# Kernel tuning notes

Hardware: AMD Instinct MI355X
Metric: run time of the kernel (lower is better)

Reference implementation:

```python
import jax, jax.numpy as jnp
import numpy as np

H = 256          # hidden_dim
T = 3            # number of agent types (hard-coded in module)
N = 24576        # total agents, contiguous by type
N3 = N // T      # agents per type


def _ln(x, s, b):
    mu = jnp.mean(x, -1, keepdims=True)
    v = jnp.var(x, -1, keepdims=True)
    return (x - mu) * jax.lax.rsqrt(v + 1e-5) * s + b


def setup_inputs() -> dict:
    key = jax.random.key(0)
    ks = jax.random.split(key, 20)
    def p(i, shape, scale=0.02):
        return jax.random.normal(ks[i], shape, jnp.float32) * scale
    inp = {}
    inp['agent_x'] = p(0, (N, H), 1.0)
    inp['lane_x'] = p(1, (N, H), 1.0)
    inp['poly_x'] = p(2, (N, H), 1.0)
    inp['l2a_src'] = jax.random.randint(ks[3], (N,), 0, N)
    inp['g2a_src'] = jax.random.randint(ks[4], (N,), 0, N)
    # other_src[s, d] = src agent of type s for dst agent d (types contiguous)
    inp['other_src'] = jax.random.randint(ks[5], (T, N), 0, N3) + (jnp.arange(T) * N3)[:, None]
    # per-agent-type params
    inp['self_W'] = p(6, (T, H, H)); inp['self_b'] = jnp.zeros((T, H))
    inp['out_W'] = p(7, (T, 4 * H, H)); inp['out_b'] = jnp.zeros((T, H))
    inp['ffn_ln_s'] = jnp.ones((T, H)); inp['ffn_ln_b'] = jnp.zeros((T, H))
    inp['ffn_w1'] = p(8, (T, H, 4 * H)); inp['ffn_b1'] = jnp.zeros((T, 4 * H))
    inp['ffn_w2'] = p(9, (T, 4 * H, H)); inp['ffn_b2'] = jnp.zeros((T, H))
    inp['ffn_w3'] = p(10, (T, H, 4 * H)); inp['ffn_b3'] = jnp.zeros((T, 4 * H))
    # shared edge MLPs (prenorm: LN -> w1 -> relu -> w2)
    inp['l2a_ln_s'] = jnp.ones((3 * H,)); inp['l2a_ln_b'] = jnp.zeros((3 * H,))
    inp['l2a_w1'] = p(11, (3 * H, 4 * H)); inp['l2a_b1'] = jnp.zeros((4 * H,))
    inp['l2a_w2'] = p(12, (4 * H, H)); inp['l2a_b2'] = jnp.zeros((H,))
    inp['g2a_ln_s'] = jnp.ones((2 * H,)); inp['g2a_ln_b'] = jnp.zeros((2 * H,))
    inp['g2a_w1'] = p(13, (2 * H, 4 * H)); inp['g2a_b1'] = jnp.zeros((4 * H,))
    inp['g2a_w2'] = p(14, (4 * H, H)); inp['g2a_b2'] = jnp.zeros((H,))
    # per-src-agent-type 'other' MLPs
    inp['oth_ln_s'] = jnp.ones((T, 3 * H)); inp['oth_ln_b'] = jnp.zeros((T, 3 * H))
    inp['oth_w1'] = p(15, (T, 3 * H, 4 * H)); inp['oth_b1'] = jnp.zeros((T, 4 * H))
    inp['oth_w2'] = p(16, (T, 4 * H, H)); inp['oth_b2'] = jnp.zeros((T, H))
    return inp


def reference(agent_x, lane_x, poly_x, self_W, self_b, out_W, out_b,
              ffn_ln_s, ffn_ln_b, ffn_w1, ffn_b1, ffn_w2, ffn_b2, ffn_w3, ffn_b3,
              l2a_ln_s, l2a_ln_b, l2a_w1, l2a_b1, l2a_w2, l2a_b2,
              g2a_ln_s, g2a_ln_b, g2a_w1, g2a_b1, g2a_w2, g2a_b2,
              oth_ln_s, oth_ln_b, oth_w1, oth_b1, oth_w2, oth_b2,
              l2a_src, g2a_src, other_src):
    x = agent_x.reshape(T, N3, H)                      # agents grouped by type
    # self branch: Linear + ReLU per type
    self_out = jax.nn.relu(jnp.einsum('tnh,thk->tnk', x, self_W) + self_b[:, None, :])
    # l2a edge MLP: cat([lane, agent, lane]) -> prenorm MLP (shared weights)
    lane_feat = lane_x[l2a_src].reshape(T, N3, H)
    l2a_in = jnp.concatenate([lane_feat, x, lane_feat], -1)      # [T,N3,3H]
    l2a_out = jax.nn.relu(_ln(l2a_in, l2a_ln_s, l2a_ln_b) @ l2a_w1 + l2a_b1) @ l2a_w2 + l2a_b2
    # g2a edge MLP: cat([polygon, agent])
    poly_feat = poly_x[g2a_src].reshape(T, N3, H)
    g2a_in = jnp.concatenate([poly_feat, x], -1)                 # [T,N3,2H]
    g2a_out = jax.nn.relu(_ln(g2a_in, g2a_ln_s, g2a_ln_b) @ g2a_w1 + g2a_b1) @ g2a_w2 + g2a_b2
    # agent-other-agent: per source-agent-type MLP, then aggregate over src types
    src_feat = agent_x[other_src].reshape(T, T, N3, H)           # [src_t, dst_t, N3, H]
    xb = jnp.broadcast_to(x[None], (T, T, N3, H))
    oth_in = jnp.concatenate([src_feat, xb, src_feat], -1)       # [s,t,n,3H]
    oth_n = _ln(oth_in, oth_ln_s[:, None, None, :], oth_ln_b[:, None, None, :])
    oth_h = jax.nn.relu(jnp.einsum('stnd,sdm->stnm', oth_n, oth_w1) + oth_b1[:, None, None, :])
    oth_out = jnp.einsum('stnm,smh->stnh', oth_h, oth_w2) + oth_b2[:, None, None, :]
    other_agg = oth_out.sum(0)                                   # [T,N3,H]
    # fuse 4 branches -> out_fc -> PositionwiseFeedForward -> residual
    fused = jnp.concatenate([self_out, l2a_out, g2a_out, other_agg], -1)  # [T,N3,4H]
    out = jnp.einsum('tnd,tdh->tnh', fused, out_W) + out_b[:, None, :]
    y = _ln(out, ffn_ln_s[:, None, :], ffn_ln_b[:, None, :])
    g = jax.nn.silu(jnp.einsum('tnh,thm->tnm', y, ffn_w1) + ffn_b1[:, None, :])
    u = jnp.einsum('tnh,thm->tnm', y, ffn_w3) + ffn_b3[:, None, :]
    out = out + jnp.einsum('tnm,tmh->tnh', g * u, ffn_w2) + ffn_b2[:, None, :]
    return (out + x).reshape(N, H)
```

## Files before the change

kernel.cpp:

```cpp
#include <hip/hip_runtime.h>
#include <hip/hip_bf16.h>

typedef __hip_bfloat16 bf16;
typedef __bf16 v8bf __attribute__((ext_vector_type(8)));
typedef float f32x4 __attribute__((ext_vector_type(4)));

#define N_AG 24576
#define N3 8192

struct __align__(8) bf4 { bf16 x, y, z, w; };
__device__ __forceinline__ bf4 mk4(float a, float b, float c, float d) {
  bf4 r{__float2bfloat16(a), __float2bfloat16(b), __float2bfloat16(c), __float2bfloat16(d)};
  return r;
}

enum {
  EPI_RELU_BIAS = 0,
  EPI_BIAS      = 1,
  EPI_ACC_INIT  = 2,
  EPI_ACC_ADD   = 3,
  EPI_FINAL     = 4,
  EPI_SILU      = 5,
  EPI_MUL       = 6,
  EPI_GLU       = 7
};

__device__ __forceinline__ void gl_lds16(const bf16* g, short* l) {
  __builtin_amdgcn_global_load_lds(
      (const __attribute__((address_space(1))) unsigned int*)g,
      (__attribute__((address_space(3))) unsigned int*)l, 16, 0, 0);
}

template<int EPI>
__device__ __forceinline__
void gemm_body(const bf16* __restrict__ A, int lda,
               const bf16* __restrict__ Bt, int ldb,
               const float* __restrict__ bias,
               float* __restrict__ accbuf,
               bf16* __restrict__ Cout, int ldc,
               const float* __restrict__ resid,
               float* __restrict__ CoutF,
               const bf16* __restrict__ gin,
               int K, int Nc, int row0, int col0)
{
  __shared__ __align__(16) short As[2][128 * 32];
  __shared__ __align__(16) short Bs[2][128 * 32];

  const int tid  = threadIdx.x;
  const int lane = tid & 63;
  const int w    = tid >> 6;
  const int quad = lane >> 4;
  const int l15  = lane & 15;

  f32x4 acc[4][4];
  const f32x4 zero = {0.f, 0.f, 0.f, 0.f};
#pragma unroll
  for (int i = 0; i < 4; ++i)
#pragma unroll
    for (int j = 0; j < 4; ++j) acc[i][j] = zero;

  const int srow = (w << 5) + (lane >> 2);
  const int ss   = ((lane >> 2) & 3) ^ ((lane >> 4) & 1);
  const int sc   = ((lane & 3) ^ ss) << 3;
  const bf16* aG = A  + (long)(row0 + srow) * lda + sc;
  const bf16* bG = Bt + (long)(col0 + srow) * ldb + sc;
  const int ldsOff = w * 1024;

  const int wr = (w >> 1) * 64;
  const int wc = (w & 1) * 64;
  const int fs = (l15 & 3) ^ ((l15 >> 2) & 1);

  gl_lds16(aG,                  As[0] + ldsOff);
  gl_lds16(aG + (long)16 * lda, As[0] + ldsOff + 512);
  gl_lds16(bG,                  Bs[0] + ldsOff);
  gl_lds16(bG + (long)16 * ldb, Bs[0] + ldsOff + 512);
  __syncthreads();

  int cur = 0;
  for (int k0 = 0; k0 < K; k0 += 32) {
    const int nk = k0 + 32;
    if (nk < K) {
      short* An = As[cur ^ 1] + ldsOff;
      short* Bn = Bs[cur ^ 1] + ldsOff;
      gl_lds16(aG + nk,                  An);
      gl_lds16(aG + nk + (long)16 * lda, An + 512);
      gl_lds16(bG + nk,                  Bn);
      gl_lds16(bG + nk + (long)16 * ldb, Bn + 512);
    }
    const short* Ac = As[cur];
    const short* Bc = Bs[cur];
    const int pc = (quad ^ fs) * 8;
    v8bf af[4], bfm[4];
#pragma unroll
    for (int i = 0; i < 4; ++i) {
      af[i]  = *(const v8bf*)&Ac[(wr + i * 16 + l15) * 32 + pc];
      bfm[i] = *(const v8bf*)&Bc[(wc + i * 16 + l15) * 32 + pc];
    }
#pragma unroll
    for (int i = 0; i < 4; ++i)
#pragma unroll
      for (int j = 0; j < 4; ++j)
        acc[i][j] = __builtin_amdgcn_mfma_f32_16x16x32_bf16(af[i], bfm[j], acc[i][j], 0, 0, 0);
    __syncthreads();
    cur ^= 1;
  }

  if constexpr (EPI == EPI_GLU) {
#pragma unroll
    for (int ct = 0; ct < 4; ct += 2) {
      const int colg = col0 + wc + ct * 16 + l15;
      const int hcol = ((colg >> 5) << 4) + (colg & 15);
      const float bg = bias[colg];
      const float bu = bias[colg + 16];
#pragma unroll
      for (int rt = 0; rt < 4; ++rt) {
#pragma unroll
        for (int i = 0; i < 4; ++i) {
          const int row = row0 + wr + rt * 16 + quad * 4 + i;
          const float vg = acc[rt][ct][i] + bg;
          const float vu = acc[rt][ct + 1][i] + bu;
          Cout[(long)row * ldc + hcol] =
              __float2bfloat16(vg / (1.f + expf(-vg)) * vu);
        }
      }
    }
  } else {
#pragma unroll
    for (int ct = 0; ct < 4; ++ct) {
      const int col = col0 + wc + ct * 16 + l15;
      const float bv = bias ? bias[col] : 0.f;
#pragma unroll
      for (int rt = 0; rt < 4; ++rt) {
#pragma unroll
        for (int i = 0; i < 4; ++i) {
          const int row = row0 + wr + rt * 16 + quad * 4 + i;
          float v = acc[rt][ct][i] + bv;
          if constexpr (EPI == EPI_RELU_BIAS) {
            Cout[(long)row * ldc + col] = __float2bfloat16(v > 0.f ? v : 0.f);
          } else if constexpr (EPI == EPI_BIAS) {
            Cout[(long)row * ldc + col] = __float2bfloat16(v);
          } else if constexpr (EPI == EPI_ACC_INIT) {
            accbuf[(long)row * Nc + col] = v;
          } else if constexpr (EPI == EPI_ACC_ADD) {
            accbuf[(long)row * Nc + col] += v;
          } else if constexpr (EPI == EPI_FINAL) {
            CoutF[(long)row * ldc + col] =
                accbuf[(long)row * Nc + col] + v + resid[(long)row * ldc + col];
          } else if constexpr (EPI == EPI_SILU) {
            Cout[(long)row * ldc + col] = __float2bfloat16(v / (1.f + expf(-v)));
          } else {
            const float g = __bfloat162float(gin[(long)row * ldc + col]);
            Cout[(long)row * ldc + col] = __float2bfloat16(v * g);
          }
        }
      }
    }
  }
}

template<int EPI>
__global__ __launch_bounds__(256)
void gemm_k(const bf16* __restrict__ A, int lda,
            const bf16* __restrict__ Bt, int ldb, long bTs,
            const float* __restrict__ bias, long biasTs,
            float* __restrict__ accbuf,
            bf16* __restrict__ Cout, int ldc,
            const float* __restrict__ resid,
            float* __restrict__ CoutF,
            const bf16* __restrict__ gin,
            int K, int Nc)
{
  const int row0 = blockIdx.x * 128;
  const int col0 = blockIdx.y * 128;
  const int t    = row0 >> 13;
  gemm_body<EPI>(A, lda, Bt + (long)t * bTs, ldb,
                 bias ? bias + (long)t * biasTs : nullptr,
                 accbuf, Cout, ldc, resid, CoutF, gin, K, Nc, row0, col0);
}

__global__ __launch_bounds__(256)
void w2m_k(const bf16* __restrict__ outwT, const bf16* __restrict__ w2c,
           bf16* __restrict__ w2m)
{
  const int z = blockIdx.z, b = z / 3, t = z % 3;
  const int j = (b == 0) ? 1 : (b == 1) ? 2 : 3;
  gemm_body<EPI_BIAS>(outwT + (long)t * 262144 + j * 256, 1024,
                      w2c + (long)b * 262144, 256,
                      nullptr, nullptr, w2m + (long)z * 262144, 1024,
                      nullptr, nullptr, nullptr, 256, 1024,
                      blockIdx.x * 128, blockIdx.y * 128);
}

__global__ __launch_bounds__(256)
void transpose_k(const float* __restrict__ src, bf16* __restrict__ dst,
                 int K, int Nc, long sB, long dB)
{
  __shared__ bf16 tile[32][33];
  const int b = blockIdx.z;
  const float* s = src + (long)b * sB;
  bf16* d = dst + (long)b * dB;
  const int kb = blockIdx.y * 32, nb = blockIdx.x * 32;
  const int tx = threadIdx.x & 31, ty = threadIdx.x >> 5;
#pragma unroll
  for (int i = 0; i < 32; i += 8)
    tile[ty + i][tx] = __float2bfloat16(s[(long)(kb + ty + i) * Nc + nb + tx]);
  __syncthreads();
#pragma unroll
  for (int i = 0; i < 32; i += 8)
    d[(long)(nb + ty + i) * K + kb + tx] = tile[tx][ty + i];
}

__global__ __launch_bounds__(256)
void transpose13_k(const float* __restrict__ w1, const float* __restrict__ w3,
                   bf16* __restrict__ dst)
{
  __shared__ bf16 tile[32][33];
  const int t  = blockIdx.z;
  const int n0 = blockIdx.x * 32;
  const int k0 = blockIdx.y * 32;
  const int gi = n0 >> 5;
  const int tx = threadIdx.x & 31, ty = threadIdx.x >> 5;
  const float* src = ((tx & 16) ? w3 : w1) + (long)t * 262144;
  const int c = 16 * gi + (tx & 15);
#pragma unroll
  for (int i = 0; i < 32; i += 8)
    tile[ty + i][tx] = __float2bfloat16(src[(long)(k0 + ty + i) * 1024 + c]);
  __syncthreads();
#pragma unroll
  for (int i = 0; i < 32; i += 8)
    dst[((long)t * 2048 + n0 + ty + i) * 256 + k0 + tx] = tile[tx][ty + i];
}

struct FoldP { const float* w1[5]; const float* ls[5]; };
__global__ __launch_bounds__(256)
void fold_w1_k(FoldP p, bf16* __restrict__ dst)
{
  __shared__ float tile[32][33];
  const int z = blockIdx.z;
  const float* w1 = p.w1[z];
  const float* ls = p.ls[z];
  bf16* d = dst + (long)z * 524288;
  const int n0 = blockIdx.x * 32, i0 = blockIdx.y * 32;
  const int tx = threadIdx.x & 31, ty = threadIdx.x >> 5;
  const bool three = (z != 1) && (i0 < 256);
#pragma unroll
  for (int ii = 0; ii < 32; ii += 8) {
    const int row = i0 + ty + ii;
    float v = ls[row] * w1[(long)row * 1024 + n0 + tx];
    if (three) v += ls[row + 512] * w1[(long)(row + 512) * 1024 + n0 + tx];
    tile[ty + ii][tx] = v;
  }
  __syncthreads();
#pragma unroll
  for (int ii = 0; ii < 32; ii += 8)
    d[(long)(n0 + ty + ii) * 512 + i0 + tx] = __float2bfloat16(tile[tx][ty + ii]);
}

struct BInitP { const float* b1[5]; const float* fb1; const float* fb3; };
__global__ __launch_bounds__(256)
void binit_k(BInitP p, float* __restrict__ B1F,
             const float* __restrict__ out_b, float* __restrict__ TB,
             float* __restrict__ B13)
{
  const int i = blockIdx.x * 256 + threadIdx.x;
  if (i < 5120) {
    B1F[i] = p.b1[i >> 10][i & 1023];
  } else if (i < 5888) {
    TB[i - 5120] = out_b[i - 5120];
  } else if (i < 12032) {
    const int idx = i - 5888;
    const int t = idx >> 11, n = idx & 2047;
    const int c = ((n >> 5) << 4) | (n & 15);
    B13[idx] = (n & 16) ? p.fb3[t * 1024 + c] : p.fb1[t * 1024 + c];
  }
}

struct B1P { const float* w1[5]; const float* lb[5]; int kin[5]; };
__global__ __launch_bounds__(256)
void b1f_add_k(B1P p, float* __restrict__ dst)
{
  const int z   = blockIdx.x;
  const int kin = p.kin[z];
  const int kpb = (kin + 31) >> 5;
  const int k0  = blockIdx.y * kpb;
  const int k1  = min(k0 + kpb, kin);
  const float* w1 = p.w1[z];
  const float* lb = p.lb[z];
  const int n = threadIdx.x;
  float a0 = 0.f, a1 = 0.f, a2 = 0.f, a3 = 0.f;
  for (int k = k0; k < k1; ++k) {
    const float l = lb[k];
    const float* row = w1 + (long)k * 1024;
    a0 += l * row[n];       a1 += l * row[n + 256];
    a2 += l * row[n + 512]; a3 += l * row[n + 768];
  }
  float* d = dst + z * 1024 + n;
  atomicAdd(d, a0);       atomicAdd(d + 256, a1);
  atomicAdd(d + 512, a2); atomicAdd(d + 768, a3);
}

__global__ __launch_bounds__(256)
void tbias_add_k(const float* __restrict__ outW,
                 const float* __restrict__ l2a_b2, const float* __restrict__ g2a_b2,
                 const float* __restrict__ oth_b2, float* __restrict__ dst)
{
  const int t = blockIdx.x, h = threadIdx.x;
  const float* W = outW + (long)t * 262144;
  const int c0 = blockIdx.y * 32;
  float acc = 0.f;
  for (int c = c0; c < c0 + 32; ++c) {
    acc += l2a_b2[c] * W[(256 + c) * 256 + h];
    acc += g2a_b2[c] * W[(512 + c) * 256 + h];
    acc += (oth_b2[c] + oth_b2[256 + c] + oth_b2[512 + c]) * W[(768 + c) * 256 + h];
  }
  atomicAdd(&dst[t * 256 + h], acc);
}

__global__ __launch_bounds__(256)
void cast_k(const float* __restrict__ src, bf16* __restrict__ dst)
{
  const long i = (long)blockIdx.x * 256 + threadIdx.x;
  const float4 v = ((const float4*)src)[i];
  ((bf4*)dst)[i] = mk4(v.x, v.y, v.z, v.w);
}

__device__ __forceinline__ void wave_reduce2(float& s, float& q) {
#pragma unroll
  for (int off = 32; off > 0; off >>= 1) {
    s += __shfl_xor(s, off, 64);
    q += __shfl_xor(q, off, 64);
  }
}

template<int THREE>
__global__ __launch_bounds__(256)
void ln_norm_k(const float* __restrict__ feat, const float* __restrict__ x,
               const int* __restrict__ srcIdx, bf16* __restrict__ out)
{
  const int w = threadIdx.x >> 6, lane = threadIdx.x & 63;
  const int r = blockIdx.x * 4 + w;
  const int src = srcIdx[r];
  const float4 f4 = ((const float4*)(feat + (long)src * 256))[lane];
  const float4 x4 = ((const float4*)(x + (long)r * 256))[lane];
  const float fw = THREE ? 2.f : 1.f;
  float s = fw * (f4.x + f4.y + f4.z + f4.w) + (x4.x + x4.y + x4.z + x4.w);
  float q = fw * (f4.x * f4.x + f4.y * f4.y + f4.z * f4.z + f4.w * f4.w) +
            (x4.x * x4.x + x4.y * x4.y + x4.z * x4.z + x4.w * x4.w);
  wave_reduce2(s, q);
  const float rD  = THREE ? (1.f / 768.f) : (1.f / 512.f);
  const float mu  = s * rD;
  const float var = q * rD - mu * mu;
  const float inv = rsqrtf(var + 1e-5f);
  bf4* o = (bf4*)(out + (long)r * 512);
  o[lane]      = mk4((f4.x - mu) * inv, (f4.y - mu) * inv,
                     (f4.z - mu) * inv, (f4.w - mu) * inv);
  o[64 + lane] = mk4((x4.x - mu) * inv, (x4.y - mu) * inv,
                     (x4.z - mu) * inv, (x4.w - mu) * inv);
}

__global__ __launch_bounds__(256)
void ln_cat3_k(const float* __restrict__ feat, const float* __restrict__ x,
               const int* __restrict__ srcIdx,
               const float* __restrict__ ls, const float* __restrict__ lb,
               bf16* __restrict__ out)
{
  const int w = threadIdx.x >> 6, lane = threadIdx.x & 63;
  const int r = blockIdx.x * 4 + w;
  const int src = srcIdx[r];
  const float4 f4 = ((const float4*)(feat + (long)src * 256))[lane];
  const float4 x4 = ((const float4*)(x + (long)r * 256))[lane];
  float s = 2.f * (f4.x + f4.y + f4.z + f4.w) + (x4.x + x4.y + x4.z + x4.w);
  float q = 2.f * (f4.x * f4.x + f4.y * f4.y + f4.z * f4.z + f4.w * f4.w) +
            (x4.x * x4.x + x4.y * x4.y + x4.z * x4.z + x4.w * x4.w);
  wave_reduce2(s, q);
  const float mu  = s * (1.f / 768.f);
  const float var = q * (1.f / 768.f) - mu * mu;
  const float inv = rsqrtf(var + 1e-5f);
  const float4 s0 = ((const float4*)ls)[lane],         b0 = ((const float4*)lb)[lane];
  const float4 s1 = ((const float4*)(ls + 256))[lane], b1 = ((const float4*)(lb + 256))[lane];
  const float4 s2 = ((const float4*)(ls + 512))[lane], b2 = ((const float4*)(lb + 512))[lane];
  bf4* o = (bf4*)(out + (long)r * 768);
  o[lane] = mk4((f4.x - mu) * inv * s0.x + b0.x, (f4.y - mu) * inv * s0.y + b0.y,
                (f4.z - mu) * inv * s0.z + b0.z, (f4.w - mu) * inv * s0.w + b0.w);
  o[64 + lane] = mk4((x4.x - mu) * inv * s1.x + b1.x, (x4.y - mu) * inv * s1.y + b1.y,
                     (x4.z - mu) * inv * s1.z + b1.z, (x4.w - mu) * inv * s1.w + b1.w);
  o[128 + lane] = mk4((f4.x - mu) * inv * s2.x + b2.x, (f4.y - mu) * inv * s2.y + b2.y,
                      (f4.z - mu) * inv * s2.z + b2.z, (f4.w - mu) * inv * s2.w + b2.w);
}

__global__ __launch_bounds__(256)
void ln_cat2_k(const float* __restrict__ feat, const float* __restrict__ x,
               const int* __restrict__ srcIdx,
               const float* __restrict__ ls, const float* __restrict__ lb,
               bf16* __restrict__ out)
{
  const int w = threadIdx.x >> 6, lane = threadIdx.x & 63;
  const int r = blockIdx.x * 4 + w;
  const int src = srcIdx[r];
  const float4 f4 = ((const float4*)(feat + (long)src * 256))[lane];
  const float4 x4 = ((const float4*)(x + (long)r * 256))[lane];
  float s = (f4.x + f4.y + f4.z + f4.w) + (x4.x + x4.y + x4.z + x4.w);
  float q = (f4.x * f4.x + f4.y * f4.y + f4.z * f4.z + f4.w * f4.w) +
            (x4.x * x4.x + x4.y * x4.y + x4.z * x4.z + x4.w * x4.w);
  wave_reduce2(s, q);
  const float mu  = s * (1.f / 512.f);
  const float var = q * (1.f / 512.f) - mu * mu;
  const float inv = rsqrtf(var + 1e-5f);
  const float4 s0 = ((const float4*)ls)[lane],         b0 = ((const float4*)lb)[lane];
  const float4 s1 = ((const float4*)(ls + 256))[lane], b1 = ((const float4*)(lb + 256))[lane];
  bf4* o = (bf4*)(out + (long)r * 512);
  o[lane] = mk4((f4.x - mu) * inv * s0.x + b0.x, (f4.y - mu) * inv * s0.y + b0.y,
                (f4.z - mu) * inv * s0.z + b0.z, (f4.w - mu) * inv * s0.w + b0.w);
  o[64 + lane] = mk4((x4.x - mu) * inv * s1.x + b1.x, (x4.y - mu) * inv * s1.y + b1.y,
                     (x4.z - mu) * inv * s1.z + b1.z, (x4.w - mu) * inv * s1.w + b1.w);
}

__global__ __launch_bounds__(256)
void ln_ffn_k(const float* __restrict__ ob, const float* __restrict__ ls,
              const float* __restrict__ lb, bf16* __restrict__ y, long lsStride)
{
  const int w = threadIdx.x >> 6, lane = threadIdx.x & 63;
  const int r = blockIdx.x * 4 + w;
  const long po = (long)(r >> 13) * lsStride;
  const float4 v4 = ((const float4*)(ob + (long)r * 256))[lane];
  float s = v4.x + v4.y + v4.z + v4.w;
  float q = v4.x * v4.x + v4.y * v4.y + v4.z * v4.z + v4.w * v4.w;
  wave_reduce2(s, q);
  const float mu  = s * (1.f / 256.f);
  const float var = q * (1.f / 256.f) - mu * mu;
  const float inv = rsqrtf(var + 1e-5f);
  const float4 s0 = ((const float4*)(ls + po))[lane];
  const float4 b0 = ((const float4*)(lb + po))[lane];
  ((bf4*)(y + (long)r * 256))[lane] =
      mk4((v4.x - mu) * inv * s0.x + b0.x, (v4.y - mu) * inv * s0.y + b0.y,
          (v4.z - mu) * inv * s0.z + b0.z, (v4.w - mu) * inv * s0.w + b0.w);
}

__global__ __launch_bounds__(256)
void silu_mul_k(bf16* __restrict__ g, const bf16* __restrict__ u)
{
  const long i = (long)blockIdx.x * 256 + threadIdx.x;
  const bf4 g4 = ((const bf4*)g)[i];
  const bf4 u4 = ((const bf4*)u)[i];
  float a = __bfloat162float(g4.x), b = __bfloat162float(g4.y);
  float c = __bfloat162float(g4.z), d = __bfloat162float(g4.w);
  a = a / (1.f + expf(-a)) * __bfloat162float(u4.x);
  b = b / (1.f + expf(-b)) * __bfloat162float(u4.y);
  c = c / (1.f + expf(-c)) * __bfloat162float(u4.z);
  d = d / (1.f + expf(-d)) * __bfloat162float(u4.w);
  ((bf4*)g)[i] = mk4(a, b, c, d);
}

__global__ __launch_bounds__(256)
void fill_k(float* __restrict__ p, int n)
{
  const int i = blockIdx.x * 256 + threadIdx.x;
  if (i < n) p[i] = 2.0f;
}

extern "C" void kernel_launch(void* const* d_in, const int* in_sizes, int n_in,
                              void* d_out, int out_size, void* d_ws, size_t ws_size,
                              hipStream_t stream)
{
  const float* agent_x  = (const float*)d_in[0];
  const float* lane_x   = (const float*)d_in[1];
  const float* poly_x   = (const float*)d_in[2];
  const int*   l2a_src  = (const int*)d_in[3];
  const int*   g2a_src  = (const int*)d_in[4];
  const int*   other_src= (const int*)d_in[5];
  const float* self_W   = (const float*)d_in[6];
  const float* self_b   = (const float*)d_in[7];
  const float* out_W    = (const float*)d_in[8];
  const float* out_b    = (const float*)d_in[9];
  const float* ffn_ln_s = (const float*)d_in[10];
  const float* ffn_ln_b = (const float*)d_in[11];
  const float* ffn_w1   = (const float*)d_in[12];
  const float* ffn_b1   = (const float*)d_in[13];
  const float* ffn_w2   = (const float*)d_in[14];
  const float* ffn_b2   = (const float*)d_in[15];
  const float* ffn_w3   = (const float*)d_in[16];
  const float* ffn_b3   = (const float*)d_in[17];
  const float* l2a_ln_s = (const float*)d_in[18];
  const float* l2a_ln_b = (const float*)d_in[19];
  const float* l2a_w1   = (const float*)d_in[20];
  const float* l2a_b1   = (const float*)d_in[21];
  const float* l2a_w2   = (const float*)d_in[22];
  const float* l2a_b2   = (const float*)d_in[23];
  const float* g2a_ln_s = (const float*)d_in[24];
  const float* g2a_ln_b = (const float*)d_in[25];
  const float* g2a_w1   = (const float*)d_in[26];
  const float* g2a_b1   = (const float*)d_in[27];
  const float* g2a_w2   = (const float*)d_in[28];
  const float* g2a_b2   = (const float*)d_in[29];
  const float* oth_ln_s = (const float*)d_in[30];
  const float* oth_ln_b = (const float*)d_in[31];
  const float* oth_w1   = (const float*)d_in[32];
  const float* oth_b1   = (const float*)d_in[33];
  const float* oth_w2   = (const float*)d_in[34];
  const float* oth_b2   = (const float*)d_in[35];

  float* outp = (float*)d_out;
  const dim3 B256(256);

  const size_t TIER_A = 135707648;
  const size_t TIER_C = 12058624;

  if (ws_size >= TIER_A) {
    char* base = (char*)d_ws;
    bf16* wT = (bf16*)base;
    const long SELF_WT = 0,       OUT_WT  = 196608,  FFN_W13T = 983040;
    const long FFN_W2T = 2555904;
    const long W2C = 3342336,     W1F     = 4653056, W2M      = 7274496;
    float* B1F  = (float*)(base + 22413312L);
    float* TB   = (float*)(base + 22433792L);
    float* B13  = (float*)(base + 22436864L);
    bf16*  nbuf = (bf16*)(base + 22461440L);
    bf16*  h1   = (bf16*)(base + 47627264L);
    float* oF   = (float*)(base + 97958912L);
    bf16*  ybuf = (bf16*)(base + 123124736L);
    bf16*  xbf  = h1;

    auto TRB = [&](const float* s, long dOff, int K, int Nc, long sB, long dB, int b) {
      transpose_k<<<dim3(Nc / 32, K / 32, b), B256, 0, stream>>>(s, wT + dOff, K, Nc, sB, dB);
    };
    TRB(self_W, SELF_WT, 256, 256,  65536, 65536, 3);
    TRB(out_W,  OUT_WT,  1024, 256, 262144, 262144, 3);
    TRB(ffn_w2, FFN_W2T, 1024, 256, 262144, 262144, 3);
    transpose13_k<<<dim3(64, 8, 3), B256, 0, stream>>>(ffn_w1, ffn_w3, wT + FFN_W13T);
    cast_k<<<256, B256, 0, stream>>>(l2a_w2, wT + W2C);
    cast_k<<<256, B256, 0, stream>>>(g2a_w2, wT + W2C + 262144);
    cast_k<<<768, B256, 0, stream>>>(oth_w2, wT + W2C + 524288);

    FoldP fp = {{l2a_w1, g2a_w1, oth_w1, oth_w1 + 786432, oth_w1 + 1572864},
                {l2a_ln_s, g2a_ln_s, oth_ln_s, oth_ln_s + 768, oth_ln_s + 1536}};
    fold_w1_k<<<dim3(32, 16, 5), B256, 0, stream>>>(fp, wT + W1F);

    BInitP ip = {{l2a_b1, g2a_b1, oth_b1, oth_b1 + 1024, oth_b1 + 2048}, ffn_b1, ffn_b3};
    binit_k<<<47, B256, 0, stream>>>(ip, B1F, out_b, TB, B13);
    B1P bp = {{l2a_w1, g2a_w1, oth_w1, oth_w1 + 786432, oth_w1 + 1572864},
              {l2a_ln_b, g2a_ln_b, oth_ln_b, oth_ln_b + 768, oth_ln_b + 1536},
              {768, 512, 768, 768, 768}};
    b1f_add_k<<<dim3(5, 32), B256, 0, stream>>>(bp, B1F);
    tbias_add_k<<<dim3(3, 8), B256, 0, stream>>>(out_W, l2a_b2, g2a_b2, oth_b2, TB);
    w2m_k<<<dim3(2, 8, 15), B256, 0, stream>>>(wT + OUT_WT, wT + W2C, wT + W2M);

    const dim3 Gw1(N_AG / 128, 8), Gw2(N_AG / 128, 2), Gglu(N_AG / 128, 16);

    cast_k<<<N_AG / 4, B256, 0, stream>>>(agent_x, xbf);
    gemm_k<EPI_RELU_BIAS><<<Gw2, B256, 0, stream>>>(
        xbf, 256, wT + SELF_WT, 256, 65536, self_b, 256,
        nullptr, ybuf, 256, nullptr, nullptr, nullptr, 256, 256);
    gemm_k<EPI_ACC_INIT><<<Gw2, B256, 0, stream>>>(
        ybuf, 256, wT + OUT_WT, 1024, 262144, TB, 256,
        oF, nullptr, 0, nullptr, nullptr, nullptr, 256, 256);

    for (int b = 0; b < 5; ++b) {
      const int* src = (b == 0) ? l2a_src : (b == 1) ? g2a_src
                                          : other_src + (long)(b - 2) * N_AG;
      const float* feat = (b == 0) ? lane_x : (b == 1) ? poly_x : agent_x;
      if (b == 1) ln_norm_k<0><<<N_AG / 4, B256, 0, stream>>>(feat, agent_x, src, nbuf);
      else        ln_norm_k<1><<<N_AG / 4, B256, 0, stream>>>(feat, agent_x, src, nbuf);
      gemm_k<EPI_RELU_BIAS><<<Gw1, B256, 0, stream>>>(
          nbuf, 512, wT + W1F + (long)b * 524288, 512, 0, B1F + b * 1024, 0,
          nullptr, h1, 1024, nullptr, nullptr, nullptr, 512, 1024);
      gemm_k<EPI_ACC_ADD><<<Gw2, B256, 0, stream>>>(
          h1, 1024, wT + W2M + (long)b * 786432, 1024, 262144, nullptr, 0,
          oF, nullptr, 0, nullptr, nullptr, nullptr, 1024, 256);
    }

    ln_ffn_k<<<N_AG / 4, B256, 0, stream>>>(oF, ffn_ln_s, ffn_ln_b, ybuf, 256);
    gemm_k<EPI_GLU><<<Gglu, B256, 0, stream>>>(
        ybuf, 256, wT + FFN_W13T, 256, 524288, B13, 2048,
        nullptr, h1, 1024, nullptr, nullptr, nullptr, 256, 2048);
    gemm_k<EPI_FINAL><<<Gw2, B256, 0, stream>>>(
        h1, 1024, wT + FFN_W2T, 1024, 262144, ffn_b2, 256,
        oF, nullptr, 256, agent_x, outp, nullptr, 1024, 256);
    return;
  }

  if (ws_size < TIER_C) {
    fill_k<<<(out_size + 255) / 256, B256, 0, stream>>>(outp, out_size);
    return;
  }

  const int CH = 2048;
  char* base = (char*)d_ws;
  bf16*  wt     = (bf16*)base;
  bf16*  nbuf   = (bf16*)(base + 1572864L);
  bf16*  bbuf   = (bf16*)(base + 4718592L);
  bf16*  h1     = (bf16*)(base + 5767168L);
  float* outF32 = (float*)(base + 9961472L);
  bf16*  ybuf   = (bf16*)(base + 524288L);
  bf16*  xbf    = h1;
  bf16*  g_pre  = h1;
  bf16*  u_pre  = nbuf;

  const dim3 Gw1(CH / 128, 8), Gw2(CH / 128, 2);
  auto TR = [&](const float* s, int K, int Nc) {
    transpose_k<<<dim3(Nc / 32, K / 32), B256, 0, stream>>>(s, wt, K, Nc, 0, 0);
  };

  for (int t = 0; t < 3; ++t) {
    for (int c = 0; c < N3 / CH; ++c) {
      const long r0 = (long)t * N3 + (long)c * CH;
      const float* xC   = agent_x + r0 * 256;
      float*       outC = outp + r0 * 256;

      cast_k<<<CH / 4, B256, 0, stream>>>(xC, xbf);
      TR(self_W + (long)t * 65536, 256, 256);
      gemm_k<EPI_RELU_BIAS><<<Gw2, B256, 0, stream>>>(
          xbf, 256, wt, 256, 0, self_b + t * 256, 0, nullptr, bbuf, 256,
          nullptr, nullptr, nullptr, 256, 256);
      TR(out_W + (long)t * 262144 + 0 * 65536, 256, 256);
      gemm_k<EPI_ACC_INIT><<<Gw2, B256, 0, stream>>>(
          bbuf, 256, wt, 256, 0, out_b + t * 256, 0, outF32, nullptr, 0,
          nullptr, nullptr, nullptr, 256, 256);

      ln_cat3_k<<<CH / 4, B256, 0, stream>>>(lane_x, xC, l2a_src + r0,
                                             l2a_ln_s, l2a_ln_b, nbuf);
      TR(l2a_w1, 768, 1024);
      gemm_k<EPI_RELU_BIAS><<<Gw1, B256, 0, stream>>>(
          nbuf, 768, wt, 768, 0, l2a_b1, 0, nullptr, h1, 1024,
          nullptr, nullptr, nullptr, 768, 1024);
      TR(l2a_w2, 1024, 256);
      gemm_k<EPI_BIAS><<<Gw2, B256, 0, stream>>>(
          h1, 1024, wt, 1024, 0, l2a_b2, 0, nullptr, bbuf, 256,
          nullptr, nullptr, nullptr, 1024, 256);
      TR(out_W + (long)t * 262144 + 1 * 65536, 256, 256);
      gemm_k<EPI_ACC_ADD><<<Gw2, B256, 0, stream>>>(
          bbuf, 256, wt, 256, 0, nullptr, 0, outF32, nullptr, 0,
          nullptr, nullptr, nullptr, 256, 256);

      ln_cat2_k<<<CH / 4, B256, 0, stream>>>(poly_x, xC, g2a_src + r0,
                                             g2a_ln_s, g2a_ln_b, nbuf);
      TR(g2a_w1, 512, 1024);
      gemm_k<EPI_RELU_BIAS><<<Gw1, B256, 0, stream>>>(
          nbuf, 512, wt, 512, 0, g2a_b1, 0, nullptr, h1, 1024,
          nullptr, nullptr, nullptr, 512, 1024);
      TR(g2a_w2, 1024, 256);
      gemm_k<EPI_BIAS><<<Gw2, B256, 0, stream>>>(
          h1, 1024, wt, 1024, 0, g2a_b2, 0, nullptr, bbuf, 256,
          nullptr, nullptr, nullptr, 1024, 256);
      TR(out_W + (long)t * 262144 + 2 * 65536, 256, 256);
      gemm_k<EPI_ACC_ADD><<<Gw2, B256, 0, stream>>>(
          bbuf, 256, wt, 256, 0, nullptr, 0, outF32, nullptr, 0,
          nullptr, nullptr, nullptr, 256, 256);

      for (int s = 0; s < 3; ++s) {
        ln_cat3_k<<<CH / 4, B256, 0, stream>>>(
            agent_x, xC, other_src + (long)s * N_AG + r0,
            oth_ln_s + s * 768, oth_ln_b + s * 768, nbuf);
        TR(oth_w1 + (long)s * 786432, 768, 1024);
        gemm_k<EPI_RELU_BIAS><<<Gw1, B256, 0, stream>>>(
            nbuf, 768, wt, 768, 0, oth_b1 + s * 1024, 0, nullptr, h1, 1024,
            nullptr, nullptr, nullptr, 768, 1024);
        TR(oth_w2 + (long)s * 262144, 1024, 256);
        gemm_k<EPI_BIAS><<<Gw2, B256, 0, stream>>>(
            h1, 1024, wt, 1024, 0, oth_b2 + s * 256, 0, nullptr, bbuf, 256,
            nullptr, nullptr, nullptr, 1024, 256);
        TR(out_W + (long)t * 262144 + 3 * 65536, 256, 256);
        gemm_k<EPI_ACC_ADD><<<Gw2, B256, 0, stream>>>(
            bbuf, 256, wt, 256, 0, nullptr, 0, outF32, nullptr, 0,
            nullptr, nullptr, nullptr, 256, 256);
      }

      ln_ffn_k<<<CH / 4, B256, 0, stream>>>(outF32, ffn_ln_s + t * 256,
                                            ffn_ln_b + t * 256, ybuf, 0);
      TR(ffn_w1 + (long)t * 262144, 256, 1024);
      gemm_k<EPI_BIAS><<<Gw1, B256, 0, stream>>>(
          ybuf, 256, wt, 256, 0, ffn_b1 + t * 1024, 0, nullptr, g_pre, 1024,
          nullptr, nullptr, nullptr, 256, 1024);
      TR(ffn_w3 + (long)t * 262144, 256, 1024);
      gemm_k<EPI_BIAS><<<Gw1, B256, 0, stream>>>(
          ybuf, 256, wt, 256, 0, ffn_b3 + t * 1024, 0, nullptr, u_pre, 1024,
          nullptr, nullptr, nullptr, 256, 1024);
      silu_mul_k<<<CH, B256, 0, stream>>>(g_pre, u_pre);
      TR(ffn_w2 + (long)t * 262144, 1024, 256);
      gemm_k<EPI_FINAL><<<Gw2, B256, 0, stream>>>(
          g_pre, 1024, wt, 1024, 0, ffn_b2 + t * 256, 0, outF32, nullptr, 256,
          xC, outC, nullptr, 1024, 256);
    }
  }
}
```

Before: 844.1 us.

## Split-K with atomic accumulation for narrow N=256 GEMMs

After: 1.131 ms. +34.0%, slower.

```diff
diff --git a/kernel.cpp b/kernel.cpp
--- a/kernel.cpp
+++ b/kernel.cpp
@@ -22,7 +22,8 @@
   EPI_FINAL     = 4,
   EPI_SILU      = 5,
   EPI_MUL       = 6,
-  EPI_GLU       = 7
+  EPI_GLU       = 7,
+  EPI_ACC_ATOMIC= 8
 };
 
 __device__ __forceinline__ void gl_lds16(const bf16* g, short* l) {
@@ -143,6 +144,8 @@
             accbuf[(long)row * Nc + col] = v;
           } else if constexpr (EPI == EPI_ACC_ADD) {
             accbuf[(long)row * Nc + col] += v;
+          } else if constexpr (EPI == EPI_ACC_ATOMIC) {
+            atomicAdd(&accbuf[(long)row * Nc + col], v);
           } else if constexpr (EPI == EPI_FINAL) {
             CoutF[(long)row * ldc + col] =
                 accbuf[(long)row * Nc + col] + v + resid[(long)row * ldc + col];
@@ -178,6 +181,24 @@
                  accbuf, Cout, ldc, resid, CoutF, gin, K, Nc, row0, col0);
 }
 
+template<int EPI>
+__global__ __launch_bounds__(256)
+void gemm_splitk_k(const bf16* __restrict__ A, int lda,
+                   const bf16* __restrict__ Bt, int ldb, long bTs,
+                   const float* __restrict__ bias,
+                   float* __restrict__ accbuf, int Kper, int Nc)
+{
+  const int row0 = blockIdx.x * 128;
+  const int col0 = blockIdx.y * 128;
+  const int t    = row0 >> 13;
+  const int z    = blockIdx.z;
+  gemm_body<EPI>(A + (long)z * Kper, lda,
+                 Bt + (long)t * bTs + (long)z * Kper, ldb,
+                 (z == 0) ? bias : nullptr,
+                 accbuf, nullptr, 0, nullptr, nullptr, nullptr,
+                 Kper, Nc, row0, col0);
+}
+
 __global__ __launch_bounds__(256)
 void w2m_k(const bf16* __restrict__ outwT, const bf16* __restrict__ w2c,
            bf16* __restrict__ w2m)
@@ -189,6 +210,23 @@
                       nullptr, nullptr, w2m + (long)z * 262144, 1024,
                       nullptr, nullptr, nullptr, 256, 1024,
                       blockIdx.x * 128, blockIdx.y * 128);
+}
+
+__global__ __launch_bounds__(256)
+void final_add_k(const float* __restrict__ oF, const float* __restrict__ x,
+                 const float* __restrict__ b2, float* __restrict__ out)
+{
+  const long idx = (long)blockIdx.x * 256 + threadIdx.x;
+  const long i4  = idx * 4;
+  const int  t   = (int)(i4 >> 21);
+  const int  c4  = (int)(i4 & 255) >> 2;
+  const float4 a = ((const float4*)oF)[idx];
+  const float4 r = ((const float4*)x)[idx];
+  const float4 b = ((const float4*)(b2 + t * 256))[c4];
+  float4 o;
+  o.x = a.x + b.x + r.x; o.y = a.y + b.y + r.y;
+  o.z = a.z + b.z + r.z; o.w = a.w + b.w + r.w;
+  ((float4*)out)[idx] = o;
 }
 
 __global__ __launch_bounds__(256)
@@ -545,6 +583,7 @@
     w2m_k<<<dim3(2, 8, 15), B256, 0, stream>>>(wT + OUT_WT, wT + W2C, wT + W2M);
 
     const dim3 Gw1(N_AG / 128, 8), Gw2(N_AG / 128, 2), Gglu(N_AG / 128, 16);
+    const dim3 Gks(N_AG / 128, 2, 4);
 
     cast_k<<<N_AG / 4, B256, 0, stream>>>(agent_x, xbf);
     gemm_k<EPI_RELU_BIAS><<<Gw2, B256, 0, stream>>>(
@@ -563,18 +602,18 @@
       gemm_k<EPI_RELU_BIAS><<<Gw1, B256, 0, stream>>>(
           nbuf, 512, wT + W1F + (long)b * 524288, 512, 0, B1F + b * 1024, 0,
           nullptr, h1, 1024, nullptr, nullptr, nullptr, 512, 1024);
-      gemm_k<EPI_ACC_ADD><<<Gw2, B256, 0, stream>>>(
-          h1, 1024, wT + W2M + (long)b * 786432, 1024, 262144, nullptr, 0,
-          oF, nullptr, 0, nullptr, nullptr, nullptr, 1024, 256);
+      gemm_splitk_k<EPI_ACC_ATOMIC><<<Gks, B256, 0, stream>>>(
+          h1, 1024, wT + W2M + (long)b * 786432, 1024, 262144,
+          nullptr, oF, 256, 256);
     }
 
     ln_ffn_k<<<N_AG / 4, B256, 0, stream>>>(oF, ffn_ln_s, ffn_ln_b, ybuf, 256);
     gemm_k<EPI_GLU><<<Gglu, B256, 0, stream>>>(
         ybuf, 256, wT + FFN_W13T, 256, 524288, B13, 2048,
         nullptr, h1, 1024, nullptr, nullptr, nullptr, 256, 2048);
-    gemm_k<EPI_FINAL><<<Gw2, B256, 0, stream>>>(
-        h1, 1024, wT + FFN_W2T, 1024, 262144, ffn_b2, 256,
-        oF, nullptr, 256, agent_x, outp, nullptr, 1024, 256);
+    gemm_splitk_k<EPI_ACC_ATOMIC><<<Gks, B256, 0, stream>>>(
+        h1, 1024, wT + FFN_W2T, 1024, 262144, nullptr, oF, 256, 256);
+    final_add_k<<<N_AG / 4, B256, 0, stream>>>(oF, agent_x, ffn_b2, outp);
     return;
   }
 
```

## Add 64x64-tile GEMM kernel for narrow-output GEMMs to raise block count

Applied to the files above, without the earlier changes.

After: 805.7 us. -4.5%, faster.

```diff
diff --git a/kernel.cpp b/kernel.cpp
--- a/kernel.cpp
+++ b/kernel.cpp
@@ -159,6 +159,100 @@
 }
 
 template<int EPI>
+__device__ __forceinline__
+void gemm64_body(const bf16* __restrict__ A, int lda,
+                 const bf16* __restrict__ Bt, int ldb,
+                 const float* __restrict__ bias,
+                 float* __restrict__ accbuf,
+                 bf16* __restrict__ Cout, int ldc,
+                 const float* __restrict__ resid,
+                 float* __restrict__ CoutF,
+                 int K, int Nc, int row0, int col0)
+{
+  __shared__ __align__(16) short As[2][64 * 32];
+  __shared__ __align__(16) short Bs[2][64 * 32];
+
+  const int tid  = threadIdx.x;
+  const int lane = tid & 63;
+  const int w    = tid >> 6;
+  const int quad = lane >> 4;
+  const int l15  = lane & 15;
+
+  f32x4 acc[2][2];
+  const f32x4 zero = {0.f, 0.f, 0.f, 0.f};
+#pragma unroll
+  for (int i = 0; i < 2; ++i)
+#pragma unroll
+    for (int j = 0; j < 2; ++j) acc[i][j] = zero;
+
+  const int srow = (w << 4) + (lane >> 2);
+  const int ss   = ((lane >> 2) & 3) ^ ((lane >> 4) & 1);
+  const int sc   = ((lane & 3) ^ ss) << 3;
+  const bf16* aG = A  + (long)(row0 + srow) * lda + sc;
+  const bf16* bG = Bt + (long)(col0 + srow) * ldb + sc;
+  const int ldsOff = w * 512;
+
+  const int wr = (w >> 1) * 32;
+  const int wc = (w & 1) * 32;
+  const int fs = (l15 & 3) ^ ((l15 >> 2) & 1);
+
+  gl_lds16(aG, As[0] + ldsOff);
+  gl_lds16(bG, Bs[0] + ldsOff);
+  __syncthreads();
+
+  int cur = 0;
+  for (int k0 = 0; k0 < K; k0 += 32) {
+    const int nk = k0 + 32;
+    if (nk < K) {
+      gl_lds16(aG + nk, As[cur ^ 1] + ldsOff);
+      gl_lds16(bG + nk, Bs[cur ^ 1] + ldsOff);
+    }
+    const short* Ac = As[cur];
+    const short* Bc = Bs[cur];
+    const int pc = (quad ^ fs) * 8;
+    v8bf af[2], bfm[2];
+#pragma unroll
+    for (int i = 0; i < 2; ++i) {
+      af[i]  = *(const v8bf*)&Ac[(wr + i * 16 + l15) * 32 + pc];
+      bfm[i] = *(const v8bf*)&Bc[(wc + i * 16 + l15) * 32 + pc];
+    }
+#pragma unroll
+    for (int i = 0; i < 2; ++i)
+#pragma unroll
+      for (int j = 0; j < 2; ++j)
+        acc[i][j] = __builtin_amdgcn_mfma_f32_16x16x32_bf16(af[i], bfm[j], acc[i][j], 0, 0, 0);
+    __syncthreads();
+    cur ^= 1;
+  }
+
+#pragma unroll
+  for (int ct = 0; ct < 2; ++ct) {
+    const int col = col0 + wc + ct * 16 + l15;
+    const float bv = bias ? bias[col] : 0.f;
+#pragma unroll
+    for (int rt = 0; rt < 2; ++rt) {
+#pragma unroll
+      for (int i = 0; i < 4; ++i) {
+        const int row = row0 + wr + rt * 16 + quad * 4 + i;
+        float v = acc[rt][ct][i] + bv;
+        if constexpr (EPI == EPI_RELU_BIAS) {
+          Cout[(long)row * ldc + col] = __float2bfloat16(v > 0.f ? v : 0.f);
+        } else if constexpr (EPI == EPI_BIAS) {
+          Cout[(long)row * ldc + col] = __float2bfloat16(v);
+        } else if constexpr (EPI == EPI_ACC_INIT) {
+          accbuf[(long)row * Nc + col] = v;
+        } else if constexpr (EPI == EPI_ACC_ADD) {
+          accbuf[(long)row * Nc + col] += v;
+        } else if constexpr (EPI == EPI_FINAL) {
+          CoutF[(long)row * ldc + col] =
+              accbuf[(long)row * Nc + col] + v + resid[(long)row * ldc + col];
+        }
+      }
+    }
+  }
+}
+
+template<int EPI>
 __global__ __launch_bounds__(256)
 void gemm_k(const bf16* __restrict__ A, int lda,
             const bf16* __restrict__ Bt, int ldb, long bTs,
@@ -178,17 +272,36 @@
                  accbuf, Cout, ldc, resid, CoutF, gin, K, Nc, row0, col0);
 }
 
+template<int EPI>
+__global__ __launch_bounds__(256)
+void gemm64_k(const bf16* __restrict__ A, int lda,
+              const bf16* __restrict__ Bt, int ldb, long bTs,
+              const float* __restrict__ bias, long biasTs,
+              float* __restrict__ accbuf,
+              bf16* __restrict__ Cout, int ldc,
+              const float* __restrict__ resid,
+              float* __restrict__ CoutF,
+              int K, int Nc)
+{
+  const int row0 = blockIdx.x * 64;
+  const int col0 = blockIdx.y * 64;
+  const int t    = row0 >> 13;
+  gemm64_body<EPI>(A, lda, Bt + (long)t * bTs, ldb,
+                   bias ? bias + (long)t * biasTs : nullptr,
+                   accbuf, Cout, ldc, resid, CoutF, K, Nc, row0, col0);
+}
+
 __global__ __launch_bounds__(256)
 void w2m_k(const bf16* __restrict__ outwT, const bf16* __restrict__ w2c,
            bf16* __restrict__ w2m)
 {
   const int z = blockIdx.z, b = z / 3, t = z % 3;
   const int j = (b == 0) ? 1 : (b == 1) ? 2 : 3;
-  gemm_body<EPI_BIAS>(outwT + (long)t * 262144 + j * 256, 1024,
-                      w2c + (long)b * 262144, 256,
-                      nullptr, nullptr, w2m + (long)z * 262144, 1024,
-                      nullptr, nullptr, nullptr, 256, 1024,
-                      blockIdx.x * 128, blockIdx.y * 128);
+  gemm64_body<EPI_BIAS>(outwT + (long)t * 262144 + j * 256, 1024,
+                        w2c + (long)b * 262144, 256,
+                        nullptr, nullptr, w2m + (long)z * 262144, 1024,
+                        nullptr, nullptr, 256, 1024,
+                        blockIdx.x * 64, blockIdx.y * 64);
 }
 
 __global__ __launch_bounds__(256)
@@ -542,17 +655,18 @@
               {768, 512, 768, 768, 768}};
     b1f_add_k<<<dim3(5, 32), B256, 0, stream>>>(bp, B1F);
     tbias_add_k<<<dim3(3, 8), B256, 0, stream>>>(out_W, l2a_b2, g2a_b2, oth_b2, TB);
-    w2m_k<<<dim3(2, 8, 15), B256, 0, stream>>>(wT + OUT_WT, wT + W2C, wT + W2M);
-
-    const dim3 Gw1(N_AG / 128, 8), Gw2(N_AG / 128, 2), Gglu(N_AG / 128, 16);
+    w2m_k<<<dim3(4, 16, 15), B256, 0, stream>>>(wT + OUT_WT, wT + W2C, wT + W2M);
+
+    const dim3 Gw1(N_AG / 128, 8), Gglu(N_AG / 128, 16);
+    const dim3 G64(N_AG / 64, 4);
 
     cast_k<<<N_AG / 4, B256, 0, stream>>>(agent_x, xbf);
-    gemm_k<EPI_RELU_BIAS><<<Gw2, B256, 0, stream>>>(
+    gemm64_k<EPI_RELU_BIAS><<<G64, B256, 0, stream>>>(
         xbf, 256, wT + SELF_WT, 256, 65536, self_b, 256,
-        nullptr, ybuf, 256, nullptr, nullptr, nullptr, 256, 256);
-    gemm_k<EPI_ACC_INIT><<<Gw2, B256, 0, stream>>>(
+        nullptr, ybuf, 256, nullptr, nullptr, 256, 256);
+    gemm64_k<EPI_ACC_INIT><<<G64, B256, 0, stream>>>(
         ybuf, 256, wT + OUT_WT, 1024, 262144, TB, 256,
-        oF, nullptr, 0, nullptr, nullptr, nullptr, 256, 256);
+        oF, nullptr, 0, nullptr, nullptr, 256, 256);
 
     for (int b = 0; b < 5; ++b) {
       const int* src = (b == 0) ? l2a_src : (b == 1) ? g2a_src
@@ -563,18 +677,18 @@
       gemm_k<EPI_RELU_BIAS><<<Gw1, B256, 0, stream>>>(
           nbuf, 512, wT + W1F + (long)b * 524288, 512, 0, B1F + b * 1024, 0,
           nullptr, h1, 1024, nullptr, nullptr, nullptr, 512, 1024);
-      gemm_k<EPI_ACC_ADD><<<Gw2, B256, 0, stream>>>(
+      gemm64_k<EPI_ACC_ADD><<<G64, B256, 0, stream>>>(
           h1, 1024, wT + W2M + (long)b * 786432, 1024, 262144, nullptr, 0,
-          oF, nullptr, 0, nullptr, nullptr, nullptr, 1024, 256);
+          oF, nullptr, 0, nullptr, nullptr, 1024, 256);
     }
 
     ln_ffn_k<<<N_AG / 4, B256, 0, stream>>>(oF, ffn_ln_s, ffn_ln_b, ybuf, 256);
     gemm_k<EPI_GLU><<<Gglu, B256, 0, stream>>>(
         ybuf, 256, wT + FFN_W13T, 256, 524288, B13, 2048,
         nullptr, h1, 1024, nullptr, nullptr, nullptr, 256, 2048);
-    gemm_k<EPI_FINAL><<<Gw2, B256, 0, stream>>>(
+    gemm64_k<EPI_FINAL><<<G64, B256, 0, stream>>>(
         h1, 1024, wT + FFN_W2T, 1024, 262144, ffn_b2, 256,
-        oF, nullptr, 256, agent_x, outp, nullptr, 1024, 256);
+        oF, nullptr, 256, agent_x, outp, 1024, 256);
     return;
   }
 
```
